# Performance work log

Hardware: AMD Instinct MI355X
Metric: run time of the kernel (lower is better)

## Reference

```python
import jax, jax.numpy as jnp
import numpy as np


def _mlp(x, W1, b1, W2, b2):
    # x: [..., 3d]; Linear weights stored torch-style: W1 [d, 3d], W2 [1, d]
    h = jax.nn.relu(jnp.einsum('...i,di->...d', x, W1) + b1)
    return jax.nn.sigmoid(jnp.einsum('...d,od->...o', h, W2) + b2)[..., 0]


def setup_inputs() -> dict:
    key = jax.random.key(0)
    ks = jax.random.split(key, 6)
    N, d, E, K = 1000000, 64, 65536, 16
    embeds = jax.random.normal(ks[0], (N, d), dtype=jnp.float32)
    pos = jax.random.randint(ks[1], (E, 2), 0, N, dtype=jnp.int64)
    neg = jax.random.randint(ks[2], (E, K, 2), 0, N, dtype=jnp.int64)
    # xavier-uniform init as in the torch module
    lim1 = float(np.sqrt(6.0 / (3 * d + d)))
    lim2 = float(np.sqrt(6.0 / (d + 1)))
    W1 = jax.random.uniform(ks[3], (d, 3 * d), jnp.float32, -lim1, lim1)
    b1 = jnp.zeros((d,), jnp.float32)
    W2 = jax.random.uniform(ks[4], (1, d), jnp.float32, -lim2, lim2)
    b2 = jnp.zeros((1,), jnp.float32)
    return {"embeds": embeds, "pos": pos, "neg": neg,
            "W1": W1, "b1": b1, "W2": W2, "b2": b2}


def reference(embeds, pos, neg, W1, b1, W2, b2):
    # positive pairs: [E, 3d]
    pu = embeds[pos[:, 0]]
    pv = embeds[pos[:, 1]]
    pos_emb = jnp.concatenate([pu, pv, pu * pv], axis=-1)
    # negative pairs: [E, K, 3d]
    nu = embeds[neg[:, :, 0]]
    nv = embeds[neg[:, :, 1]]
    neg_emb = jnp.concatenate([nu, nv, nu * nv], axis=-1)
    pos_scr = jnp.exp(_mlp(pos_emb, W1, b1, W2, b2))          # [E]
    neg_scr = jnp.exp(_mlp(neg_emb, W1, b1, W2, b2))          # [E, K]
    denom = jnp.sum(neg_scr, axis=-1) + pos_scr               # [E]
    loss = -jnp.sum(pos_scr / (denom + 1e-8) + 1e-8)
    return loss
```

## Files before the change

### kernel.cpp

```cpp
#include <hip/hip_runtime.h>
#include <math.h>

#define N_EMB   1000000
#define D       64
#define E_PAIRS 65536
#define K_NEG   16
#define P_TOTAL (E_PAIRS * (K_NEG + 1))
#define PPB     128
#define XS      200

typedef __attribute__((ext_vector_type(8))) short  short8;
typedef __attribute__((ext_vector_type(4))) float  float4v;

static __device__ __forceinline__ unsigned short f2bf(float f) {
    unsigned int x = __float_as_uint(f);
    unsigned int r = (x + 0x7fffu + ((x >> 16) & 1u)) >> 16;
    return (unsigned short)r;
}

__global__ __launch_bounds__(256)
void prep_kernel(const float* __restrict__ W1, unsigned short* __restrict__ W1bf)
{
    int i = blockIdx.x * 256 + threadIdx.x;
    if (i < 64 * 192) W1bf[i] = f2bf(W1[i]);
}

__global__ __launch_bounds__(256, 3)
void score_kernel(const float* __restrict__ embeds,
                  const int*   __restrict__ pos,
                  const int*   __restrict__ neg,
                  const unsigned short* __restrict__ W1bf,
                  const float* __restrict__ b1,
                  const float* __restrict__ W2,
                  const float* __restrict__ b2,
                  float*       __restrict__ scores)
{
    __shared__ unsigned short X[PPB * XS];
    __shared__ int uidx[PPB];
    __shared__ int vidx[PPB];

    const int t = threadIdx.x;
    const int pbase = blockIdx.x * PPB;

    if (t < PPB) {
        int p = pbase + t;
        int ui, vi;
        if (p < E_PAIRS) {
            ui = pos[2 * p];
            vi = pos[2 * p + 1];
        } else {
            int q = p - E_PAIRS;
            ui = neg[2 * q];
            vi = neg[2 * q + 1];
        }
        uidx[t] = ui;
        vidx[t] = vi;
    }
    __syncthreads();

    const int seg = t & 15;
    #pragma unroll
    for (int it = 0; it < 8; ++it) {
        int pr = it * 16 + (t >> 4);
        int ui = uidx[pr], vi = vidx[pr];
        float4 u4 = *(const float4*)(embeds + (long long)ui * D + seg * 4);
        float4 v4 = *(const float4*)(embeds + (long long)vi * D + seg * 4);
        float4 w4 = make_float4(u4.x * v4.x, u4.y * v4.y, u4.z * v4.z, u4.w * v4.w);

        union { unsigned short s[4]; uint2 v; } pu, pv, pw;
        pu.s[0] = f2bf(u4.x); pu.s[1] = f2bf(u4.y); pu.s[2] = f2bf(u4.z); pu.s[3] = f2bf(u4.w);
        pv.s[0] = f2bf(v4.x); pv.s[1] = f2bf(v4.y); pv.s[2] = f2bf(v4.z); pv.s[3] = f2bf(v4.w);
        pw.s[0] = f2bf(w4.x); pw.s[1] = f2bf(w4.y); pw.s[2] = f2bf(w4.z); pw.s[3] = f2bf(w4.w);

        unsigned short* xp = X + pr * XS + seg * 4;
        *(uint2*)(xp)       = pu.v;
        *(uint2*)(xp + 64)  = pv.v;
        *(uint2*)(xp + 128) = pw.v;
    }
    __syncthreads();

    const int lane = t & 63;
    const int wave = t >> 6;
    const int c16  = lane & 15;
    const int quad = lane >> 4;
    const int wp0  = wave * 32;

    float4v acc[2][4];
    #pragma unroll
    for (int mt = 0; mt < 2; ++mt)
        #pragma unroll
        for (int nt = 0; nt < 4; ++nt)
            acc[mt][nt] = (float4v){0.f, 0.f, 0.f, 0.f};

    #pragma unroll
    for (int ks = 0; ks < 6; ++ks) {
        const int koff = ks * 32 + quad * 8;
        short8 a0 = *(const short8*)(X + (wp0 + c16) * XS + koff);
        short8 a1 = *(const short8*)(X + (wp0 + 16 + c16) * XS + koff);
        short8 bfrag[4];
        #pragma unroll
        for (int nt = 0; nt < 4; ++nt)
            bfrag[nt] = *(const short8*)(W1bf + (nt * 16 + c16) * 192 + koff);
        #pragma unroll
        for (int nt = 0; nt < 4; ++nt) {
            acc[0][nt] = __builtin_amdgcn_mfma_f32_16x16x32_bf16(a0, bfrag[nt], acc[0][nt], 0, 0, 0);
            acc[1][nt] = __builtin_amdgcn_mfma_f32_16x16x32_bf16(a1, bfrag[nt], acc[1][nt], 0, 0, 0);
        }
    }

    float b1v[4], w2v[4];
    #pragma unroll
    for (int nt = 0; nt < 4; ++nt) {
        b1v[nt] = b1[nt * 16 + c16];
        w2v[nt] = W2[nt * 16 + c16];
    }
    const float b2v = b2[0];

    #pragma unroll
    for (int mt = 0; mt < 2; ++mt) {
        #pragma unroll
        for (int reg = 0; reg < 4; ++reg) {
            float s = 0.f;
            #pragma unroll
            for (int nt = 0; nt < 4; ++nt) {
                float h = acc[mt][nt][reg] + b1v[nt];
                s += (h > 0.f ? h : 0.f) * w2v[nt];
            }
            s += __shfl_xor(s, 1);
            s += __shfl_xor(s, 2);
            s += __shfl_xor(s, 4);
            s += __shfl_xor(s, 8);
            if (c16 == 0) {
                float sig = 1.f / (1.f + expf(-(s + b2v)));
                scores[pbase + wp0 + mt * 16 + quad * 4 + reg] = expf(sig);
            }
        }
    }
}

__global__ __launch_bounds__(256)
void reduce_kernel(const float* __restrict__ scores, float* __restrict__ partials)
{
    __shared__ float sdata[256];
    int e = blockIdx.x * 256 + threadIdx.x;
    float pos_s = scores[e];
    const float* ns = scores + E_PAIRS + (size_t)e * K_NEG;
    float nsum = 0.f;
    #pragma unroll
    for (int c = 0; c < 4; ++c) {
        float4 v = *(const float4*)(ns + c * 4);
        nsum += v.x + v.y + v.z + v.w;
    }
    float term = pos_s / (pos_s + nsum + 1e-8f) + 1e-8f;
    sdata[threadIdx.x] = term;
    __syncthreads();
    for (int s = 128; s > 0; s >>= 1) {
        if (threadIdx.x < s) sdata[threadIdx.x] += sdata[threadIdx.x + s];
        __syncthreads();
    }
    if (threadIdx.x == 0) partials[blockIdx.x] = sdata[0];
}

__global__ __launch_bounds__(256)
void final_kernel(const float* __restrict__ partials, float* __restrict__ out)
{
    __shared__ float sdata[256];
    sdata[threadIdx.x] = partials[threadIdx.x];
    __syncthreads();
    for (int s = 128; s > 0; s >>= 1) {
        if (threadIdx.x < s) sdata[threadIdx.x] += sdata[threadIdx.x + s];
        __syncthreads();
    }
    if (threadIdx.x == 0) out[0] = -sdata[0];
}

extern "C" void kernel_launch(void* const* d_in, const int* in_sizes, int n_in,
                              void* d_out, int out_size, void* d_ws, size_t ws_size,
                              hipStream_t stream)
{
    const float* embeds = (const float*)d_in[0];
    const int*   pos    = (const int*)d_in[1];
    const int*   neg    = (const int*)d_in[2];
    const float* W1     = (const float*)d_in[3];
    const float* b1     = (const float*)d_in[4];
    const float* W2     = (const float*)d_in[5];
    const float* b2     = (const float*)d_in[6];
    float* out = (float*)d_out;

    float* scores   = (float*)d_ws;
    float* partials = scores + P_TOTAL;
    unsigned short* W1bf = (unsigned short*)(partials + 256);

    prep_kernel<<<48, 256, 0, stream>>>(W1, W1bf);
    score_kernel<<<P_TOTAL / PPB, 256, 0, stream>>>(embeds, pos, neg, W1bf, b1, W2, b2, scores);
    reduce_kernel<<<E_PAIRS / 256, 256, 0, stream>>>(scores, partials);
    final_kernel<<<1, 256, 0, stream>>>(partials, out);
}
```

Before: 476.5 us.

## Load embedding rows directly into MFMA A-fragments, removing LDS staging

Each lane now gathers the u and v embedding slices it needs for its MFMA A operands straight from global memory. It builds the u, v and u*v bf16 fragments in registers instead of writing a 128x192 tile to shared memory and reading it back. This removes the LDS buffer and both block-wide barriers, and the occupancy hint rises from 3 to 4 blocks per CU. In exchange, each lane issues 32-byte reads at stride inside a row rather than fully coalesced 16-lane row reads, and register pressure grows because six fragments per row tile stay live.

```diff
diff --git a/kernel.cpp b/kernel.cpp
--- a/kernel.cpp
+++ b/kernel.cpp
@@ -7,7 +7,6 @@
 #define K_NEG   16
 #define P_TOTAL (E_PAIRS * (K_NEG + 1))
 #define PPB     128
-#define XS      200
 
 typedef __attribute__((ext_vector_type(8))) short  short8;
 typedef __attribute__((ext_vector_type(4))) float  float4v;
@@ -18,6 +17,41 @@
     return (unsigned short)r;
 }
 
+static __device__ __forceinline__ short8 pack8(float4 a, float4 b) {
+    short8 r;
+    r[0] = (short)f2bf(a.x); r[1] = (short)f2bf(a.y);
+    r[2] = (short)f2bf(a.z); r[3] = (short)f2bf(a.w);
+    r[4] = (short)f2bf(b.x); r[5] = (short)f2bf(b.y);
+    r[6] = (short)f2bf(b.z); r[7] = (short)f2bf(b.w);
+    return r;
+}
+
+static __device__ __forceinline__ float4 mul4(float4 a, float4 b) {
+    return make_float4(a.x * b.x, a.y * b.y, a.z * b.z, a.w * b.w);
+}
+
+static __device__ __forceinline__ void load_frags(const float* __restrict__ embeds,
+                                                  int ui, int vi, int quad,
+                                                  short8* fr)
+{
+    const float* up = embeds + (long long)ui * D + quad * 8;
+    const float* vp = embeds + (long long)vi * D + quad * 8;
+    float4 ua = *(const float4*)(up);
+    float4 ub = *(const float4*)(up + 4);
+    float4 uc = *(const float4*)(up + 32);
+    float4 ud = *(const float4*)(up + 36);
+    float4 va = *(const float4*)(vp);
+    float4 vb = *(const float4*)(vp + 4);
+    float4 vc = *(const float4*)(vp + 32);
+    float4 vd = *(const float4*)(vp + 36);
+    fr[0] = pack8(ua, ub);
+    fr[1] = pack8(uc, ud);
+    fr[2] = pack8(va, vb);
+    fr[3] = pack8(vc, vd);
+    fr[4] = pack8(mul4(ua, va), mul4(ub, vb));
+    fr[5] = pack8(mul4(uc, vc), mul4(ud, vd));
+}
+
 __global__ __launch_bounds__(256)
 void prep_kernel(const float* __restrict__ W1, unsigned short* __restrict__ W1bf)
 {
@@ -25,7 +59,7 @@
     if (i < 64 * 192) W1bf[i] = f2bf(W1[i]);
 }
 
-__global__ __launch_bounds__(256, 3)
+__global__ __launch_bounds__(256, 4)
 void score_kernel(const float* __restrict__ embeds,
                   const int*   __restrict__ pos,
                   const int*   __restrict__ neg,
@@ -35,55 +69,27 @@
                   const float* __restrict__ b2,
                   float*       __restrict__ scores)
 {
-    __shared__ unsigned short X[PPB * XS];
-    __shared__ int uidx[PPB];
-    __shared__ int vidx[PPB];
-
-    const int t = threadIdx.x;
-    const int pbase = blockIdx.x * PPB;
-
-    if (t < PPB) {
-        int p = pbase + t;
-        int ui, vi;
-        if (p < E_PAIRS) {
-            ui = pos[2 * p];
-            vi = pos[2 * p + 1];
-        } else {
-            int q = p - E_PAIRS;
-            ui = neg[2 * q];
-            vi = neg[2 * q + 1];
-        }
-        uidx[t] = ui;
-        vidx[t] = vi;
-    }
-    __syncthreads();
-
-    const int seg = t & 15;
-    #pragma unroll
-    for (int it = 0; it < 8; ++it) {
-        int pr = it * 16 + (t >> 4);
-        int ui = uidx[pr], vi = vidx[pr];
-        float4 u4 = *(const float4*)(embeds + (long long)ui * D + seg * 4);
-        float4 v4 = *(const float4*)(embeds + (long long)vi * D + seg * 4);
-        float4 w4 = make_float4(u4.x * v4.x, u4.y * v4.y, u4.z * v4.z, u4.w * v4.w);
-
-        union { unsigned short s[4]; uint2 v; } pu, pv, pw;
-        pu.s[0] = f2bf(u4.x); pu.s[1] = f2bf(u4.y); pu.s[2] = f2bf(u4.z); pu.s[3] = f2bf(u4.w);
-        pv.s[0] = f2bf(v4.x); pv.s[1] = f2bf(v4.y); pv.s[2] = f2bf(v4.z); pv.s[3] = f2bf(v4.w);
-        pw.s[0] = f2bf(w4.x); pw.s[1] = f2bf(w4.y); pw.s[2] = f2bf(w4.z); pw.s[3] = f2bf(w4.w);
-
-        unsigned short* xp = X + pr * XS + seg * 4;
-        *(uint2*)(xp)       = pu.v;
-        *(uint2*)(xp + 64)  = pv.v;
-        *(uint2*)(xp + 128) = pw.v;
-    }
-    __syncthreads();
-
+    const int t    = threadIdx.x;
     const int lane = t & 63;
     const int wave = t >> 6;
     const int c16  = lane & 15;
     const int quad = lane >> 4;
-    const int wp0  = wave * 32;
+    const int pw   = blockIdx.x * PPB + wave * 32;
+
+    const int p0 = pw + c16;
+    const int p1 = pw + 16 + c16;
+    int2 i0, i1;
+    if (pw < E_PAIRS) {
+        i0 = ((const int2*)pos)[p0];
+        i1 = ((const int2*)pos)[p1];
+    } else {
+        i0 = ((const int2*)neg)[p0 - E_PAIRS];
+        i1 = ((const int2*)neg)[p1 - E_PAIRS];
+    }
+
+    short8 a0[6], a1[6];
+    load_frags(embeds, i0.x, i0.y, quad, a0);
+    load_frags(embeds, i1.x, i1.y, quad, a1);
 
     float4v acc[2][4];
     #pragma unroll
@@ -95,16 +101,14 @@
     #pragma unroll
     for (int ks = 0; ks < 6; ++ks) {
         const int koff = ks * 32 + quad * 8;
-        short8 a0 = *(const short8*)(X + (wp0 + c16) * XS + koff);
-        short8 a1 = *(const short8*)(X + (wp0 + 16 + c16) * XS + koff);
         short8 bfrag[4];
         #pragma unroll
         for (int nt = 0; nt < 4; ++nt)
             bfrag[nt] = *(const short8*)(W1bf + (nt * 16 + c16) * 192 + koff);
         #pragma unroll
         for (int nt = 0; nt < 4; ++nt) {
-            acc[0][nt] = __builtin_amdgcn_mfma_f32_16x16x32_bf16(a0, bfrag[nt], acc[0][nt], 0, 0, 0);
-            acc[1][nt] = __builtin_amdgcn_mfma_f32_16x16x32_bf16(a1, bfrag[nt], acc[1][nt], 0, 0, 0);
+            acc[0][nt] = __builtin_amdgcn_mfma_f32_16x16x32_bf16(a0[ks], bfrag[nt], acc[0][nt], 0, 0, 0);
+            acc[1][nt] = __builtin_amdgcn_mfma_f32_16x16x32_bf16(a1[ks], bfrag[nt], acc[1][nt], 0, 0, 0);
         }
     }
 
@@ -132,7 +136,7 @@
             s += __shfl_xor(s, 8);
             if (c16 == 0) {
                 float sig = 1.f / (1.f + expf(-(s + b2v)));
-                scores[pbase + wp0 + mt * 16 + quad * 4 + reg] = expf(sig);
+                scores[pw + mt * 16 + quad * 4 + reg] = expf(sig);
             }
         }
     }
```

Result: no change. 469.8 us (-1.4%).
